# Optimization experiments

Hardware: AMD Instinct MI355X
Metric: run time of the kernel (lower is better)

The kernel has to match this reference:

```python
import jax, jax.numpy as jnp
import numpy as np

NUM_EXPERTS = 8
TOP_K = 2
HIDDEN = 1024
INTER = 4096
LB_WEIGHT = 0.01


def setup_inputs() -> dict:
    key = jax.random.key(0)
    ks = jax.random.split(key, 6)
    s = 0.02
    return {
        "hidden_states": jax.random.normal(ks[0], (2, 2048, HIDDEN), dtype=jnp.float32),
        "Wg": jax.random.normal(ks[1], (HIDDEN, NUM_EXPERTS), dtype=jnp.float32) * s,
        "w1": jax.random.normal(ks[2], (NUM_EXPERTS, HIDDEN, INTER), dtype=jnp.float32) * s,
        "b1": jnp.zeros((NUM_EXPERTS, INTER), dtype=jnp.float32),
        "w2": jax.random.normal(ks[3], (NUM_EXPERTS, INTER, HIDDEN), dtype=jnp.float32) * s,
        "b2": jnp.zeros((NUM_EXPERTS, HIDDEN), dtype=jnp.float32),
    }


def reference(hidden_states, Wg, w1, b1, w2, b2):
    B, S, H = hidden_states.shape
    x = hidden_states.reshape(-1, H)            # [T, H]
    T = x.shape[0]

    # 1. Gating: softmax over experts, top-k selection, renormalized gates
    probs = jax.nn.softmax(x @ Wg, axis=-1)     # [T, E]
    top_v, top_i = jax.lax.top_k(probs, TOP_K)  # [T, K]
    gate = top_v / jnp.sum(top_v, axis=-1, keepdims=True)

    # Load-balancing aux loss: E * sum(frac_assigned * mean_prob) * weight
    frac = jnp.mean(jax.nn.one_hot(top_i, NUM_EXPERTS, dtype=probs.dtype), axis=(0, 1))  # [E]
    mean_p = jnp.mean(probs, axis=0)            # [E]
    aux_loss = NUM_EXPERTS * jnp.sum(frac * mean_p) * LB_WEIGHT

    # Combine weights: per-token weight for each expert (sum of matching top-k gates)
    combine = jnp.zeros((T, NUM_EXPERTS), dtype=x.dtype)
    combine = combine.at[jnp.arange(T)[:, None], top_i].add(gate)  # [T, E]

    # 2-4. Expert FFN + weighted combine (math-equivalent dense-per-expert form)
    out = jnp.zeros_like(x)
    for e in range(NUM_EXPERTS):
        h = jax.nn.gelu(x @ w1[e] + b1[e])       # [T, INTER]
        out = out + combine[:, e:e + 1] * (h @ w2[e] + b2[e])
    return out.reshape(B, S, H), aux_loss
```

## Files before the change

### kernel.cpp

```cpp
#include <hip/hip_runtime.h>
#include <hip/hip_bf16.h>

#define T_TOK   4096
#define HID     1024
#define INTER   4096
#define NEXP    8
#define MAXT    72
#define MAXSLOT 9216
#define TPB_TOK 16

typedef __attribute__((ext_vector_type(8))) short s16x8;
typedef __attribute__((ext_vector_type(4))) float f32x4;

__device__ __forceinline__ void load_lds16(const void* g, void* l) {
    __builtin_amdgcn_global_load_lds(
        (const __attribute__((address_space(1))) void*)g,
        (__attribute__((address_space(3))) void*)l, 16, 0, 0);
}

__device__ __forceinline__ float gelu_tanh(float v) {
    float c = 0.7978845608028654f;
    float u = v + 0.044715f * v * v * v;
    return 0.5f * v * (1.0f + tanhf(c * u));
}

__global__ void transpose_bf16_kernel(const float* __restrict__ in, __hip_bfloat16* __restrict__ out,
                                      int R, int C) {
    __shared__ float tile[32][33];
    size_t eoff = (size_t)blockIdx.z * R * C;
    int c0 = blockIdx.x * 32, r0 = blockIdx.y * 32;
    int tx = threadIdx.x & 31, ty = threadIdx.x >> 5;
    #pragma unroll
    for (int i = 0; i < 32; i += 8)
        tile[ty + i][tx] = in[eoff + (size_t)(r0 + ty + i) * C + c0 + tx];
    __syncthreads();
    #pragma unroll
    for (int i = 0; i < 32; i += 8)
        out[eoff + (size_t)(c0 + ty + i) * R + r0 + tx] = __float2bfloat16(tile[tx][ty + i]);
}

__global__ void gating_kernel(const float* __restrict__ x, const float* __restrict__ Wg,
                              __hip_bfloat16* __restrict__ xb,
                              float* __restrict__ combine, int* __restrict__ counts,
                              float* __restrict__ prob_sums, int* __restrict__ idxcap) {
    __shared__ float s_ps[NEXP];
    __shared__ int   s_cnt[NEXP];
    __shared__ int   s_base[NEXP];
    __shared__ int   s_ei[TPB_TOK][2];
    __shared__ int   s_rk[TPB_TOK][2];

    int tid = threadIdx.x, wv = tid >> 6, ln = tid & 63;
    if (tid < NEXP) { s_ps[tid] = 0.f; s_cnt[tid] = 0; }
    __syncthreads();

    int t0 = blockIdx.x * TPB_TOK;
    for (int sub = 0; sub < 4; ++sub) {
        int tl = wv * 4 + sub;
        int t = t0 + tl;
        const float* xr = x + (size_t)t * HID + ln * 16;
        float4 xv[4];
        #pragma unroll
        for (int i = 0; i < 4; ++i) xv[i] = *(const float4*)(xr + i * 4);

        __hip_bfloat16 row[16];
        #pragma unroll
        for (int i = 0; i < 4; ++i) {
            row[i * 4 + 0] = __float2bfloat16(xv[i].x);
            row[i * 4 + 1] = __float2bfloat16(xv[i].y);
            row[i * 4 + 2] = __float2bfloat16(xv[i].z);
            row[i * 4 + 3] = __float2bfloat16(xv[i].w);
        }
        __hip_bfloat16* xbr = xb + (size_t)t * HID + ln * 16;
        *(s16x8*)(xbr)     = *(s16x8*)&row[0];
        *(s16x8*)(xbr + 8) = *(s16x8*)&row[8];

        float acc[NEXP] = {0,0,0,0,0,0,0,0};
        #pragma unroll
        for (int i = 0; i < 4; ++i) {
            float xs[4] = {xv[i].x, xv[i].y, xv[i].z, xv[i].w};
            #pragma unroll
            for (int j = 0; j < 4; ++j) {
                int k = ln * 16 + i * 4 + j;
                float4 wa = *(const float4*)(Wg + (size_t)k * 8);
                float4 wb = *(const float4*)(Wg + (size_t)k * 8 + 4);
                acc[0] += xs[j] * wa.x; acc[1] += xs[j] * wa.y;
                acc[2] += xs[j] * wa.z; acc[3] += xs[j] * wa.w;
                acc[4] += xs[j] * wb.x; acc[5] += xs[j] * wb.y;
                acc[6] += xs[j] * wb.z; acc[7] += xs[j] * wb.w;
            }
        }
        #pragma unroll
        for (int e = 0; e < NEXP; ++e)
            #pragma unroll
            for (int off = 32; off >= 1; off >>= 1)
                acc[e] += __shfl_xor(acc[e], off);

        float m = acc[0];
        #pragma unroll
        for (int e = 1; e < NEXP; ++e) m = fmaxf(m, acc[e]);
        float p[NEXP], s = 0.f;
        #pragma unroll
        for (int e = 0; e < NEXP; ++e) { p[e] = __expf(acc[e] - m); s += p[e]; }
        float inv = 1.0f / s;
        #pragma unroll
        for (int e = 0; e < NEXP; ++e) p[e] *= inv;

        int i0 = 0;
        #pragma unroll
        for (int e = 1; e < NEXP; ++e) if (p[e] > p[i0]) i0 = e;
        int i1 = (i0 == 0) ? 1 : 0;
        #pragma unroll
        for (int e = 0; e < NEXP; ++e) if (e != i0 && p[e] > p[i1]) i1 = e;
        float gs = p[i0] + p[i1];
        float g0 = p[i0] / gs, g1 = p[i1] / gs;

        if (ln == 0) {
            float rowc[NEXP] = {0,0,0,0,0,0,0,0};
            rowc[i0] = g0; rowc[i1] = g1;
            float4* cr = (float4*)(combine + (size_t)t * NEXP);
            cr[0] = make_float4(rowc[0], rowc[1], rowc[2], rowc[3]);
            cr[1] = make_float4(rowc[4], rowc[5], rowc[6], rowc[7]);
            #pragma unroll
            for (int e = 0; e < NEXP; ++e) atomicAdd(&s_ps[e], p[e]);
            int r0 = atomicAdd(&s_cnt[i0], 1);
            int r1 = atomicAdd(&s_cnt[i1], 1);
            s_ei[tl][0] = i0; s_rk[tl][0] = r0;
            s_ei[tl][1] = i1; s_rk[tl][1] = r1;
        }
    }
    __syncthreads();
    if (tid < NEXP) {
        s_base[tid] = atomicAdd(&counts[tid], s_cnt[tid]);
        atomicAdd(&prob_sums[tid], s_ps[tid]);
    }
    __syncthreads();
    if (tid < TPB_TOK * 2) {
        int tl = tid >> 1, k = tid & 1;
        int e = s_ei[tl][k];
        idxcap[e * T_TOK + s_base[e] + s_rk[tl][k]] = t0 + tl;
    }
}

__global__ void plan_kernel(const int* __restrict__ counts, const float* __restrict__ prob_sums,
                            int* __restrict__ offs, int* __restrict__ tile_e,
                            int* __restrict__ tile_s0, int* __restrict__ tile_nv,
                            int* __restrict__ ntiles, float* __restrict__ aux_out) {
    int tt = 0, o = 0;
    for (int e = 0; e < NEXP; ++e) {
        offs[e] = o;
        int n = counts[e];
        int nt = (n + 127) >> 7;
        for (int r = 0; r < nt; ++r) {
            tile_e[tt] = e;
            tile_s0[tt] = o + r * 128;
            int nv = n - r * 128; if (nv > 128) nv = 128;
            tile_nv[tt] = nv;
            ++tt;
        }
        o += nt * 128;
    }
    *ntiles = tt;
    float aux = 0.f;
    for (int e = 0; e < NEXP; ++e)
        aux += ((float)counts[e] / (float)(T_TOK * 2)) * (prob_sums[e] / (float)T_TOK);
    aux_out[0] = (float)NEXP * aux * 0.01f;
}

__global__ void compact_kernel(const int* __restrict__ counts, const int* __restrict__ offs,
                               const int* __restrict__ tile_e, const int* __restrict__ tile_s0,
                               const int* __restrict__ ntiles,
                               const int* __restrict__ idxcap, int* __restrict__ idxc) {
    int tt = blockIdx.x;
    if (tt >= *ntiles) return;
    int e = tile_e[tt];
    int slot = tile_s0[tt] + threadIdx.x;
    int i = slot - offs[e];
    int n = counts[e];
    idxc[slot] = (i < n) ? idxcap[e * T_TOK + i] : 0;
}


__global__ __launch_bounds__(256, 2)
void gemm1_kernel(const __hip_bfloat16* __restrict__ xb,
                  const __hip_bfloat16* __restrict__ w1b,
                  const float* __restrict__ b1,
                  const int* __restrict__ idxc,
                  const int* __restrict__ tile_e, const int* __restrict__ tile_s0,
                  const int* __restrict__ ntiles,
                  __hip_bfloat16* __restrict__ h)
{
    const int NWG = MAXT * (INTER / 128);
    int bid = blockIdx.x;
    int w = (bid & 7) * (NWG / 8) + (bid >> 3);
    int tt = w >> 5;
    int n0 = (w & 31) * 128;
    if (tt >= *ntiles) return;
    int e = tile_e[tt];
    int slot0 = tile_s0[tt];

    __shared__ __hip_bfloat16 As[128][64];
    __shared__ __hip_bfloat16 Bs[128][64];
    __shared__ int s_idx[128];

    int tid = threadIdx.x, wv = tid >> 6, ln = tid & 63;
    if (tid < 128) s_idx[tid] = idxc[slot0 + tid];
    __syncthreads();

    int swz = ((ln & 7) ^ (ln >> 3)) * 8;
    const __hip_bfloat16* srcA[4];
    const __hip_bfloat16* srcB[4];
    const __hip_bfloat16* wbase = w1b + (size_t)e * INTER * HID;
    #pragma unroll
    for (int j = 0; j < 4; ++j) {
        int r = wv * 32 + j * 8 + (ln >> 3);
        srcA[j] = xb + (size_t)s_idx[r] * HID + swz;
        srcB[j] = wbase + (size_t)(n0 + r) * HID + swz;
    }

    f32x4 acc[4][4] = {};
    int wr = wv >> 1, wc = wv & 1, lr = ln & 15;

    for (int kt = 0; kt < HID; kt += 64) {
        #pragma unroll
        for (int j = 0; j < 4; ++j) {
            load_lds16(srcA[j] + kt, (void*)&As[wv * 32 + j * 8][0]);
            load_lds16(srcB[j] + kt, (void*)&Bs[wv * 32 + j * 8][0]);
        }
        __syncthreads();
        #pragma unroll
        for (int kk = 0; kk < 2; ++kk) {
            int lslot = (((kk * 4) + (ln >> 4)) ^ (ln & 7)) * 16;
            s16x8 af[4], bf[4];
            #pragma unroll
            for (int m = 0; m < 4; ++m) {
                int row = wr * 64 + m * 16 + lr;
                af[m] = *(const s16x8*)((const char*)&As[0][0] + row * 128 + lslot);
            }
            #pragma unroll
            for (int n = 0; n < 4; ++n) {
                int row = wc * 64 + n * 16 + lr;
                bf[n] = *(const s16x8*)((const char*)&Bs[0][0] + row * 128 + lslot);
            }
            #pragma unroll
            for (int m = 0; m < 4; ++m)
                #pragma unroll
                for (int n = 0; n < 4; ++n)
                    acc[m][n] = __builtin_amdgcn_mfma_f32_16x16x32_bf16(af[m], bf[n], acc[m][n], 0, 0, 0);
        }
        __syncthreads();
    }

    const float* b1e = b1 + (size_t)e * INTER;
    int rq = (ln >> 4) * 4;
    #pragma unroll
    for (int m = 0; m < 4; ++m) {
        #pragma unroll
        for (int r = 0; r < 4; ++r) {
            int row = wr * 64 + m * 16 + rq + r;
            size_t hrow = (size_t)(slot0 + row) * INTER;
            #pragma unroll
            for (int n = 0; n < 4; ++n) {
                int col = n0 + wc * 64 + n * 16 + lr;
                float v = acc[m][n][r] + b1e[col];
                h[hrow + col] = __float2bfloat16(gelu_tanh(v));
            }
        }
    }
}

__global__ __launch_bounds__(256, 2)
void gemm2_kernel(const __hip_bfloat16* __restrict__ h,
                  const __hip_bfloat16* __restrict__ w2b,
                  const float* __restrict__ b2,
                  const float* __restrict__ combine,
                  const int* __restrict__ idxc,
                  const int* __restrict__ tile_e, const int* __restrict__ tile_s0,
                  const int* __restrict__ tile_nv, const int* __restrict__ ntiles,
                  float* __restrict__ out)
{
    const int NWG = MAXT * (HID / 128) * 2;
    int bid = blockIdx.x;
    int w = (bid & 7) * (NWG / 8) + (bid >> 3);
    int ks = w & 1;
    int n0 = ((w >> 1) & 7) * 128;
    int tt = w >> 4;
    if (tt >= *ntiles) return;
    int e = tile_e[tt];
    int slot0 = tile_s0[tt];

    __shared__ __hip_bfloat16 As[128][64];
    __shared__ __hip_bfloat16 Bs[128][64];
    __shared__ int s_idx[128];

    int tid = threadIdx.x, wv = tid >> 6, ln = tid & 63;
    if (tid < 128) s_idx[tid] = idxc[slot0 + tid];

    int swz = ((ln & 7) ^ (ln >> 3)) * 8;
    const __hip_bfloat16* srcA[4];
    const __hip_bfloat16* srcB[4];
    const __hip_bfloat16* wbase = w2b + (size_t)e * HID * INTER;
    #pragma unroll
    for (int j = 0; j < 4; ++j) {
        int r = wv * 32 + j * 8 + (ln >> 3);
        srcA[j] = h + (size_t)(slot0 + r) * INTER + swz;
        srcB[j] = wbase + (size_t)(n0 + r) * INTER + swz;
    }

    f32x4 acc[4][4] = {};
    int wr = wv >> 1, wc = wv & 1, lr = ln & 15;

    int k0 = ks * (INTER / 2), k1 = k0 + INTER / 2;
    for (int kt = k0; kt < k1; kt += 64) {
        #pragma unroll
        for (int j = 0; j < 4; ++j) {
            load_lds16(srcA[j] + kt, (void*)&As[wv * 32 + j * 8][0]);
            load_lds16(srcB[j] + kt, (void*)&Bs[wv * 32 + j * 8][0]);
        }
        __syncthreads();
        #pragma unroll
        for (int kk = 0; kk < 2; ++kk) {
            int lslot = (((kk * 4) + (ln >> 4)) ^ (ln & 7)) * 16;
            s16x8 af[4], bf[4];
            #pragma unroll
            for (int m = 0; m < 4; ++m) {
                int row = wr * 64 + m * 16 + lr;
                af[m] = *(const s16x8*)((const char*)&As[0][0] + row * 128 + lslot);
            }
            #pragma unroll
            for (int n = 0; n < 4; ++n) {
                int row = wc * 64 + n * 16 + lr;
                bf[n] = *(const s16x8*)((const char*)&Bs[0][0] + row * 128 + lslot);
            }
            #pragma unroll
            for (int m = 0; m < 4; ++m)
                #pragma unroll
                for (int n = 0; n < 4; ++n)
                    acc[m][n] = __builtin_amdgcn_mfma_f32_16x16x32_bf16(af[m], bf[n], acc[m][n], 0, 0, 0);
        }
        __syncthreads();
    }

    const float* b2e = b2 + (size_t)e * HID;
    int nv = tile_nv[tt];
    int rq = (ln >> 4) * 4;
    #pragma unroll
    for (int m = 0; m < 4; ++m) {
        #pragma unroll
        for (int r = 0; r < 4; ++r) {
            int row = wr * 64 + m * 16 + rq + r;
            if (row < nv) {
                int tok = s_idx[row];
                float g = combine[(size_t)tok * 8 + e];
                #pragma unroll
                for (int n = 0; n < 4; ++n) {
                    int col = n0 + wc * 64 + n * 16 + lr;
                    float v = acc[m][n][r] + (ks == 0 ? b2e[col] : 0.f);
                    atomicAdd(&out[(size_t)tok * HID + col], g * v);
                }
            }
        }
    }
}

static const size_t OFF_XB      = 0;
static const size_t SZ_XB       = (size_t)T_TOK * HID * 2;
static const size_t OFF_W1B     = OFF_XB + SZ_XB;
static const size_t SZ_W        = (size_t)NEXP * INTER * HID * 2;
static const size_t OFF_W2B     = OFF_W1B + SZ_W;
static const size_t OFF_H       = OFF_W2B + SZ_W;
static const size_t SZ_H        = (size_t)MAXSLOT * INTER * 2;
static const size_t OFF_COMBINE = OFF_H + SZ_H;
static const size_t OFF_IDXCAP  = OFF_COMBINE + (size_t)T_TOK * 8 * 4;
static const size_t OFF_IDXC    = OFF_IDXCAP + (size_t)NEXP * T_TOK * 4;
static const size_t OFF_COUNTS  = OFF_IDXC + (size_t)MAXSLOT * 4;
static const size_t OFF_PSUMS   = OFF_COUNTS + 32;
static const size_t OFF_OFFS    = OFF_PSUMS + 32;
static const size_t OFF_TILE_E  = OFF_OFFS + 64;
static const size_t OFF_TILE_S0 = OFF_TILE_E + 512;
static const size_t OFF_TILE_NV = OFF_TILE_S0 + 512;
static const size_t OFF_NTILES  = OFF_TILE_NV + 512;

extern "C" void kernel_launch(void* const* d_in, const int* in_sizes, int n_in,
                              void* d_out, int out_size, void* d_ws, size_t ws_size,
                              hipStream_t stream) {
    const float* x  = (const float*)d_in[0];
    const float* Wg = (const float*)d_in[1];
    const float* w1 = (const float*)d_in[2];
    const float* b1 = (const float*)d_in[3];
    const float* w2 = (const float*)d_in[4];
    const float* b2 = (const float*)d_in[5];
    float* out = (float*)d_out;
    char* ws = (char*)d_ws;

    __hip_bfloat16* xb   = (__hip_bfloat16*)(ws + OFF_XB);
    __hip_bfloat16* w1b  = (__hip_bfloat16*)(ws + OFF_W1B);
    __hip_bfloat16* w2b  = (__hip_bfloat16*)(ws + OFF_W2B);
    __hip_bfloat16* h    = (__hip_bfloat16*)(ws + OFF_H);
    float* combine       = (float*)(ws + OFF_COMBINE);
    int*   idxcap        = (int*)(ws + OFF_IDXCAP);
    int*   idxc          = (int*)(ws + OFF_IDXC);
    int*   counts        = (int*)(ws + OFF_COUNTS);
    float* psums         = (float*)(ws + OFF_PSUMS);
    int*   offs          = (int*)(ws + OFF_OFFS);
    int*   tile_e        = (int*)(ws + OFF_TILE_E);
    int*   tile_s0       = (int*)(ws + OFF_TILE_S0);
    int*   tile_nv       = (int*)(ws + OFF_TILE_NV);
    int*   ntiles        = (int*)(ws + OFF_NTILES);

    (void)hipMemsetAsync(out, 0, (size_t)out_size * sizeof(float), stream);
    (void)hipMemsetAsync(ws + OFF_COUNTS, 0, 64, stream);

    transpose_bf16_kernel<<<dim3(INTER / 32, HID / 32, NEXP), 256, 0, stream>>>(w1, w1b, HID, INTER);
    transpose_bf16_kernel<<<dim3(HID / 32, INTER / 32, NEXP), 256, 0, stream>>>(w2, w2b, INTER, HID);
    gating_kernel<<<T_TOK / TPB_TOK, 256, 0, stream>>>(x, Wg, xb, combine, counts, psums, idxcap);
    plan_kernel<<<1, 1, 0, stream>>>(counts, psums, offs, tile_e, tile_s0, tile_nv, ntiles,
                                     out + (size_t)T_TOK * HID);
    compact_kernel<<<MAXT, 128, 0, stream>>>(counts, offs, tile_e, tile_s0, ntiles, idxcap, idxc);
    gemm1_kernel<<<MAXT * (INTER / 128), 256, 0, stream>>>(xb, w1b, b1, idxc, tile_e, tile_s0,
                                                           ntiles, h);
    gemm2_kernel<<<MAXT * (HID / 128) * 2, 256, 0, stream>>>(h, w2b, b2, combine, idxc, tile_e,
                                                             tile_s0, tile_nv, ntiles, out);
}
```

Before: 382.8 us.

## Vectorize weight transpose with 64x64 tiles, cheaper GELU, raise GEMM occupancy

The weight transpose now uses 64x64 tiles with float4 loads and 16-byte bf16 stores, aimed at the bandwidth-bound fp32-to-bf16 conversion of w1 and w2 (about 268 MB read). GELU's tanh is rewritten as x*sigmoid(2z) using __expf to shorten the epilogue. GEMM launch bounds go from 2 to 3 waves per SIMD, which can force register spills. A missing __syncthreads after the s_idx load in gemm2 is added, and the gating row buffer gets 16-byte alignment.

```diff
diff --git a/kernel.cpp b/kernel.cpp
--- a/kernel.cpp
+++ b/kernel.cpp
@@ -20,23 +20,38 @@
 
 __device__ __forceinline__ float gelu_tanh(float v) {
     float c = 0.7978845608028654f;
-    float u = v + 0.044715f * v * v * v;
-    return 0.5f * v * (1.0f + tanhf(c * u));
+    float z = c * (v + 0.044715f * v * v * v);
+    return v / (1.0f + __expf(-2.0f * z));
 }
 
 __global__ void transpose_bf16_kernel(const float* __restrict__ in, __hip_bfloat16* __restrict__ out,
                                       int R, int C) {
-    __shared__ float tile[32][33];
+    __shared__ float tile[64][65];
     size_t eoff = (size_t)blockIdx.z * R * C;
-    int c0 = blockIdx.x * 32, r0 = blockIdx.y * 32;
-    int tx = threadIdx.x & 31, ty = threadIdx.x >> 5;
-    #pragma unroll
-    for (int i = 0; i < 32; i += 8)
-        tile[ty + i][tx] = in[eoff + (size_t)(r0 + ty + i) * C + c0 + tx];
-    __syncthreads();
-    #pragma unroll
-    for (int i = 0; i < 32; i += 8)
-        out[eoff + (size_t)(c0 + ty + i) * R + r0 + tx] = __float2bfloat16(tile[tx][ty + i]);
+    int c0 = blockIdx.x * 64, r0 = blockIdx.y * 64;
+    int tid = threadIdx.x;
+
+    int lr = tid >> 4;
+    int lc = (tid & 15) * 4;
+    #pragma unroll
+    for (int it = 0; it < 4; ++it) {
+        int r = it * 16 + lr;
+        float4 v = *(const float4*)(in + eoff + (size_t)(r0 + r) * C + c0 + lc);
+        tile[r][lc + 0] = v.x; tile[r][lc + 1] = v.y;
+        tile[r][lc + 2] = v.z; tile[r][lc + 3] = v.w;
+    }
+    __syncthreads();
+
+    int oc = tid >> 3;
+    int r8 = (tid & 7) * 8;
+    #pragma unroll
+    for (int it = 0; it < 2; ++it) {
+        int c = it * 32 + oc;
+        alignas(16) __hip_bfloat16 o[8];
+        #pragma unroll
+        for (int j = 0; j < 8; ++j) o[j] = __float2bfloat16(tile[r8 + j][c]);
+        *(s16x8*)(out + eoff + (size_t)(c0 + c) * R + r0 + r8) = *(const s16x8*)o;
+    }
 }
 
 __global__ void gating_kernel(const float* __restrict__ x, const float* __restrict__ Wg,
@@ -62,7 +77,7 @@
         #pragma unroll
         for (int i = 0; i < 4; ++i) xv[i] = *(const float4*)(xr + i * 4);
 
-        __hip_bfloat16 row[16];
+        alignas(16) __hip_bfloat16 row[16];
         #pragma unroll
         for (int i = 0; i < 4; ++i) {
             row[i * 4 + 0] = __float2bfloat16(xv[i].x);
@@ -180,7 +195,7 @@
 }
 
 
-__global__ __launch_bounds__(256, 2)
+__global__ __launch_bounds__(256, 3)
 void gemm1_kernel(const __hip_bfloat16* __restrict__ xb,
                   const __hip_bfloat16* __restrict__ w1b,
                   const float* __restrict__ b1,
@@ -268,7 +283,7 @@
     }
 }
 
-__global__ __launch_bounds__(256, 2)
+__global__ __launch_bounds__(256, 3)
 void gemm2_kernel(const __hip_bfloat16* __restrict__ h,
                   const __hip_bfloat16* __restrict__ w2b,
                   const float* __restrict__ b2,
@@ -294,6 +309,7 @@
 
     int tid = threadIdx.x, wv = tid >> 6, ln = tid & 63;
     if (tid < 128) s_idx[tid] = idxc[slot0 + tid];
+    __syncthreads();
 
     int swz = ((ln & 7) ^ (ln >> 3)) * 8;
     const __hip_bfloat16* srcA[4];
@@ -410,8 +426,8 @@
     (void)hipMemsetAsync(out, 0, (size_t)out_size * sizeof(float), stream);
     (void)hipMemsetAsync(ws + OFF_COUNTS, 0, 64, stream);
 
-    transpose_bf16_kernel<<<dim3(INTER / 32, HID / 32, NEXP), 256, 0, stream>>>(w1, w1b, HID, INTER);
-    transpose_bf16_kernel<<<dim3(HID / 32, INTER / 32, NEXP), 256, 0, stream>>>(w2, w2b, INTER, HID);
+    transpose_bf16_kernel<<<dim3(INTER / 64, HID / 64, NEXP), 256, 0, stream>>>(w1, w1b, HID, INTER);
+    transpose_bf16_kernel<<<dim3(HID / 64, INTER / 64, NEXP), 256, 0, stream>>>(w2, w2b, INTER, HID);
     gating_kernel<<<T_TOK / TPB_TOK, 256, 0, stream>>>(x, Wg, xb, combine, counts, psums, idxcap);
     plan_kernel<<<1, 1, 0, stream>>>(counts, psums, offs, tile_e, tile_s0, tile_nv, ntiles,
                                      out + (size_t)T_TOK * HID);
```

After: 370.2 us. 3.3% less time.
